# Kernel optimization log

Hardware: AMD Instinct MI355X
Metric: run time of the kernel (lower is better)

## Reference

```python
import jax, jax.numpy as jnp
import numpy as np
from jax import lax

B_, C_, H_, W_ = 4, 128, 64, 64
D_INNER, D_STATE, DT_RANK, D_CONV = 256, 16, 8, 4


def setup_inputs() -> dict:
    ks = jax.random.split(jax.random.key(0), 12)
    def rn(k, shape, fan_in):
        return jax.random.normal(k, shape, jnp.float32) * (fan_in ** -0.5)
    return {
        "x": jax.random.normal(ks[0], (B_, C_, H_, W_), jnp.float32),
        "proj_w": rn(ks[1], (C_, C_), C_),
        "in_proj_w": rn(ks[2], (2 * D_INNER, C_), C_),
        "conv_w": rn(ks[3], (D_INNER, 1, D_CONV), D_CONV),
        "conv_b": jax.random.normal(ks[4], (D_INNER,), jnp.float32) * 0.02,
        "x_proj_w": rn(ks[5], (DT_RANK + 2 * D_STATE, D_INNER), D_INNER),
        "dt_proj_w": rn(ks[6], (D_INNER, DT_RANK), DT_RANK),
        "dt_proj_b": jax.random.normal(ks[7], (D_INNER,), jnp.float32) * 0.1,
        "A_log": jax.random.uniform(ks[8], (D_INNER, D_STATE), jnp.float32),
        "D": jax.random.normal(ks[9], (D_INNER,), jnp.float32),
        "out_proj_w": rn(ks[10], (C_, D_INNER), D_INNER),
    }


def _mamba2d(x, proj_w, in_proj_w, conv_w, conv_b, x_proj_w, dt_proj_w, dt_proj_b, A_log, D, out_proj_w):
    b, c, h, w = x.shape
    L = h * w
    # 1x1 conv projection then flatten to sequence (b, L, c)
    u = jnp.einsum('oc,bchw->bohw', proj_w, x).reshape(b, c, L).transpose(0, 2, 1)
    # in_proj -> x, z gates
    xz = u @ in_proj_w.T                      # (b, L, 2*d_inner)
    xs, zg = xz[..., :D_INNER], xz[..., D_INNER:]
    # causal depthwise conv1d over sequence
    xt = xs.transpose(0, 2, 1)                # (b, d_inner, L)
    xt = lax.conv_general_dilated(xt, conv_w, window_strides=(1,),
                                  padding=[(D_CONV - 1, 0)],
                                  feature_group_count=D_INNER)
    xc = jax.nn.silu(xt + conv_b[None, :, None]).transpose(0, 2, 1)  # (b, L, d_inner)
    # input-dependent SSM params
    x_dbl = xc @ x_proj_w.T                   # (b, L, dt_rank + 2*d_state)
    dt_r = x_dbl[..., :DT_RANK]
    Bm = x_dbl[..., DT_RANK:DT_RANK + D_STATE]
    Cm = x_dbl[..., DT_RANK + D_STATE:]
    delta = jax.nn.softplus(dt_r @ dt_proj_w.T + dt_proj_b)  # (b, L, d_inner)
    A = -jnp.exp(A_log)                       # (d_inner, d_state)

    def step(hprev, inp):
        dt_t, B_t, C_t, x_t = inp             # (b,d), (b,n), (b,n), (b,d)
        dA = jnp.exp(dt_t[:, :, None] * A)    # (b, d, n)
        hn = dA * hprev + (dt_t * x_t)[:, :, None] * B_t[:, None, :]
        y = jnp.einsum('bdn,bn->bd', hn, C_t)
        return hn, y

    h0 = jnp.zeros((b, D_INNER, D_STATE), xc.dtype)
    _, ys = lax.scan(step, h0, (delta.transpose(1, 0, 2), Bm.transpose(1, 0, 2),
                                Cm.transpose(1, 0, 2), xc.transpose(1, 0, 2)))
    y = ys.transpose(1, 0, 2) + xc * D        # (b, L, d_inner) + skip
    y = y * jax.nn.silu(zg)                   # output gating
    out = y @ out_proj_w.T                    # (b, L, c)
    return out.transpose(0, 2, 1).reshape(b, c, h, w) + x


def reference(x, proj_w, in_proj_w, conv_w, conv_b, x_proj_w, dt_proj_w, dt_proj_b, A_log, D, out_proj_w):
    return _mamba2d(x, proj_w, in_proj_w, conv_w, conv_b, x_proj_w, dt_proj_w, dt_proj_b, A_log, D, out_proj_w)
```

## Files before the change

### kernel.cpp

```cpp
#include <hip/hip_runtime.h>


#define NCHUNK 128
#define CLEN 32

using s16x8 = __attribute__((ext_vector_type(8))) short;
using f32x4 = __attribute__((ext_vector_type(4))) float;

__device__ inline unsigned short f2bf(float f) {
  unsigned u = __float_as_uint(f);
  u = u + 0x7FFF + ((u >> 16) & 1);
  return (unsigned short)(u >> 16);
}

__global__ void prep_kernel(const float* __restrict__ proj_w,
                            const float* __restrict__ in_proj_w,
                            const float* __restrict__ x_proj_w,
                            const float* __restrict__ out_proj_w,
                            const float* __restrict__ A_log,
                            unsigned short* __restrict__ W2b,
                            unsigned short* __restrict__ wTb48,
                            unsigned short* __restrict__ Woutb,
                            float* __restrict__ Aneg) {
  int idx = blockIdx.x * blockDim.x + threadIdx.x;
  if (idx < 65536) {
    int o = idx >> 7, c = idx & 127;
    float acc = 0.f;
    #pragma unroll 4
    for (int i = 0; i < 128; ++i)
      acc += in_proj_w[o * 128 + i] * proj_w[i * 128 + c];
    W2b[idx] = f2bf(acc);
  } else if (idx < 65536 + 12288) {
    int t = idx - 65536;
    int j = t >> 8, k = t & 255;
    wTb48[t] = (j < 40) ? f2bf(x_proj_w[j * 256 + k]) : (unsigned short)0;
  } else if (idx < 65536 + 12288 + 32768) {
    int t = idx - (65536 + 12288);
    Woutb[t] = f2bf(out_proj_w[t]);
  } else if (idx < 65536 + 12288 + 32768 + 4096) {
    int t = idx - (65536 + 12288 + 32768);
    Aneg[t] = -__expf(A_log[t]);
  }
}

__global__ __launch_bounds__(256, 1) void gemm_xz_kernel(
    const float* __restrict__ x, const unsigned short* __restrict__ W2b,
    float* __restrict__ xz) {
  __shared__ __align__(16) unsigned short At[128 * 128];
  __shared__ __align__(16) unsigned short Bt[256 * 128];
  int m0 = (blockIdx.x >> 1) * 128;
  int o0 = (blockIdx.x & 1) * 256;
  int b  = m0 >> 12;
  int l0 = m0 & 4095;
  int t = threadIdx.x;
  #pragma unroll
  for (int j = 0; j < 16; ++j) {
    int flat = t + j * 256;
    int cr = flat >> 5, lq = (flat & 31) << 2;
    float4 v = *reinterpret_cast<const float4*>(
        &x[((size_t)(b * 128 + cr)) * 4096 + l0 + lq]);
    float vv[4] = {v.x, v.y, v.z, v.w};
    #pragma unroll
    for (int e = 0; e < 4; ++e) {
      int l = lq + e;
      int g = (cr >> 3) ^ ((l & 7) << 1);
      At[l * 128 + g * 8 + (cr & 7)] = f2bf(vv[e]);
    }
  }
  #pragma unroll
  for (int j = 0; j < 16; ++j) {
    int flat = t + j * 256;
    int row = flat >> 4, gB = flat & 15;
    s16x8 v = *reinterpret_cast<const s16x8*>(&W2b[(size_t)(o0 + row) * 128 + gB * 8]);
    int g = gB ^ ((row & 7) << 1);
    *reinterpret_cast<s16x8*>(&Bt[row * 128 + g * 8]) = v;
  }
  __syncthreads();
  int ln = t & 63, wave = t >> 6;
  int wm = wave & 1, wn = wave >> 1;
  f32x4 acc[4][8] = {};
  #pragma unroll
  for (int ks = 0; ks < 4; ++ks) {
    int gk = ks * 4 + (ln >> 4);
    s16x8 a[4], bb[8];
    #pragma unroll
    for (int mi = 0; mi < 4; ++mi) {
      int lr = wm * 64 + mi * 16 + (ln & 15);
      a[mi] = *reinterpret_cast<const s16x8*>(&At[lr * 128 + (gk ^ ((lr & 7) << 1)) * 8]);
    }
    #pragma unroll
    for (int ni = 0; ni < 8; ++ni) {
      int orow = wn * 128 + ni * 16 + (ln & 15);
      bb[ni] = *reinterpret_cast<const s16x8*>(&Bt[orow * 128 + (gk ^ ((orow & 7) << 1)) * 8]);
    }
    #pragma unroll
    for (int mi = 0; mi < 4; ++mi)
      #pragma unroll
      for (int ni = 0; ni < 8; ++ni)
        acc[mi][ni] = __builtin_amdgcn_mfma_f32_16x16x32_bf16(a[mi], bb[ni], acc[mi][ni], 0, 0, 0);
  }
  #pragma unroll
  for (int mi = 0; mi < 4; ++mi)
    #pragma unroll
    for (int ni = 0; ni < 8; ++ni)
      #pragma unroll
      for (int r = 0; r < 4; ++r) {
        int row = wm * 64 + mi * 16 + (ln >> 4) * 4 + r;
        int col = wn * 128 + ni * 16 + (ln & 15);
        xz[(size_t)(m0 + row) * 512 + o0 + col] = acc[mi][ni][r];
      }
}

__global__ __launch_bounds__(256) void conv_silu_kernel(
    const float* __restrict__ xz, const float* __restrict__ conv_w,
    const float* __restrict__ conv_b, float* __restrict__ xc,
    unsigned short* __restrict__ xcb) {
  int bl0 = blockIdx.x * 8;
  int d = threadIdx.x;
  int l0 = bl0 & 4095;
  float w0 = conv_w[d * 4 + 0], w1 = conv_w[d * 4 + 1];
  float w2 = conv_w[d * 4 + 2], w3 = conv_w[d * 4 + 3];
  float cb = conv_b[d];
  float xm1 = (l0 >= 1) ? xz[(size_t)(bl0 - 1) * 512 + d] : 0.f;
  float xm2 = (l0 >= 2) ? xz[(size_t)(bl0 - 2) * 512 + d] : 0.f;
  float xm3 = (l0 >= 3) ? xz[(size_t)(bl0 - 3) * 512 + d] : 0.f;
  #pragma unroll
  for (int r = 0; r < 8; ++r) {
    size_t bl = bl0 + r;
    float x0 = xz[bl * 512 + d];
    float acc = cb + w3 * x0 + w2 * xm1 + w1 * xm2 + w0 * xm3;
    float s = acc * (1.f / (1.f + __expf(-acc)));
    xc[bl * 256 + d] = s;
    xcb[bl * 256 + d] = f2bf(s);
    xm3 = xm2; xm2 = xm1; xm1 = x0;
  }
}

__global__ __launch_bounds__(256) void xdbl_mfma_kernel(
    const unsigned short* __restrict__ xcb, const unsigned short* __restrict__ wTb48,
    float* __restrict__ xdbl48) {
  __shared__ __align__(16) unsigned short At[64 * 256];
  __shared__ __align__(16) unsigned short Bt[48 * 256];
  int m0 = blockIdx.x * 64;
  int t = threadIdx.x;
  #pragma unroll
  for (int it = 0; it < 8; ++it) {
    int f = t + it * 256;
    int row = f >> 5, g0 = f & 31;
    s16x8 v = *reinterpret_cast<const s16x8*>(&xcb[(size_t)(m0 + row) * 256 + g0 * 8]);
    int g = g0 ^ ((row & 7) << 1);
    *reinterpret_cast<s16x8*>(&At[row * 256 + g * 8]) = v;
  }
  #pragma unroll
  for (int it = 0; it < 6; ++it) {
    int f = t + it * 256;
    int row = f >> 5, g0 = f & 31;
    s16x8 v = *reinterpret_cast<const s16x8*>(&wTb48[(size_t)row * 256 + g0 * 8]);
    int g = g0 ^ ((row & 7) << 1);
    *reinterpret_cast<s16x8*>(&Bt[row * 256 + g * 8]) = v;
  }
  __syncthreads();
  int ln = t & 63, wm = t >> 6;
  f32x4 acc[3] = {};
  #pragma unroll
  for (int ks = 0; ks < 8; ++ks) {
    int gk = ks * 4 + (ln >> 4);
    int ar = wm * 16 + (ln & 15);
    s16x8 a = *reinterpret_cast<const s16x8*>(&At[ar * 256 + (gk ^ ((ar & 7) << 1)) * 8]);
    #pragma unroll
    for (int nt = 0; nt < 3; ++nt) {
      int br = nt * 16 + (ln & 15);
      s16x8 bb = *reinterpret_cast<const s16x8*>(&Bt[br * 256 + (gk ^ ((br & 7) << 1)) * 8]);
      acc[nt] = __builtin_amdgcn_mfma_f32_16x16x32_bf16(a, bb, acc[nt], 0, 0, 0);
    }
  }
  #pragma unroll
  for (int nt = 0; nt < 3; ++nt)
    #pragma unroll
    for (int r = 0; r < 4; ++r) {
      int row = m0 + wm * 16 + (ln >> 4) * 4 + r;
      xdbl48[(size_t)row * 48 + nt * 16 + (ln & 15)] = acc[nt][r];
    }
}

__global__ __launch_bounds__(256) void scan1_kernel(
    const float* __restrict__ xc, const float* __restrict__ xdbl48,
    const float* __restrict__ dt_proj_w, const float* __restrict__ dt_proj_b,
    const float* __restrict__ Aneg,
    float* __restrict__ Ssum, float* __restrict__ chH) {
  __shared__ __align__(16) float lBC[CLEN][32];
  __shared__ __align__(16) float sdtr[CLEN][8];
  int bc = blockIdx.x;
  int b = bc >> 7;
  int bl0 = bc * 32;
  int tid = threadIdx.x;
  {
    int t0 = tid >> 3, q = (tid & 7) << 2;
    *reinterpret_cast<float4*>(&lBC[t0][q]) =
        *reinterpret_cast<const float4*>(&xdbl48[(size_t)(bl0 + t0) * 48 + 8 + q]);
    if (tid < 64) {
      int t1 = tid >> 1, q1 = (tid & 1) << 2;
      *reinterpret_cast<float4*>(&sdtr[t1][q1]) =
          *reinterpret_cast<const float4*>(&xdbl48[(size_t)(bl0 + t1) * 48 + q1]);
    }
  }
  int d = tid;
  float wrow[8];
  *reinterpret_cast<float4*>(&wrow[0]) =
      *reinterpret_cast<const float4*>(&dt_proj_w[d * 8]);
  *reinterpret_cast<float4*>(&wrow[4]) =
      *reinterpret_cast<const float4*>(&dt_proj_w[d * 8 + 4]);
  float bb = dt_proj_b[d];
  float An[16];
  #pragma unroll
  for (int q = 0; q < 4; ++q)
    *reinterpret_cast<float4*>(&An[q * 4]) =
        *reinterpret_cast<const float4*>(&Aneg[d * 16 + q * 4]);
  float xv[CLEN];
  #pragma unroll
  for (int t = 0; t < CLEN; ++t)
    xv[t] = xc[(size_t)(bl0 + t) * 256 + d];
  __syncthreads();
  float h[16] = {};
  float S = 0.f;
  #pragma unroll
  for (int t = 0; t < CLEN; ++t) {
    float a = bb;
    #pragma unroll
    for (int q = 0; q < 8; ++q) a += sdtr[t][q] * wrow[q];
    float dlv = fmaxf(a, 0.f) + __logf(1.f + __expf(-fabsf(a)));
    S += dlv;
    float dlx = dlv * xv[t];
    float4 B0 = *reinterpret_cast<const float4*>(&lBC[t][0]);
    float4 B1 = *reinterpret_cast<const float4*>(&lBC[t][4]);
    float4 B2 = *reinterpret_cast<const float4*>(&lBC[t][8]);
    float4 B3 = *reinterpret_cast<const float4*>(&lBC[t][12]);
    float Bv[16] = {B0.x,B0.y,B0.z,B0.w,B1.x,B1.y,B1.z,B1.w,
                    B2.x,B2.y,B2.z,B2.w,B3.x,B3.y,B3.z,B3.w};
    #pragma unroll
    for (int n = 0; n < 16; ++n)
      h[n] = __expf(dlv * An[n]) * h[n] + dlx * Bv[n];
  }
  int c = bc & 127;
  int p = b * 256 + d;
  Ssum[c * 1024 + p] = S;
  size_t base = ((size_t)(c * 1024 + p)) * 16;
  #pragma unroll
  for (int q = 0; q < 4; ++q) {
    float4 v{h[q*4+0], h[q*4+1], h[q*4+2], h[q*4+3]};
    *reinterpret_cast<float4*>(&chH[base + q * 4]) = v;
  }
}

__global__ void scan2_kernel(const float* __restrict__ Aneg,
                             const float* __restrict__ Ssum,
                             const float* __restrict__ chH,
                             float* __restrict__ chS) {
  int q = blockIdx.x * blockDim.x + threadIdx.x;
  int p = q >> 4, n = q & 15;
  int d = p & 255;
  float An = Aneg[d * 16 + n];
  float h = 0.f;
  #pragma unroll 8
  for (int c = 0; c < NCHUNK; ++c) {
    size_t idx = ((size_t)(c * 1024 + p)) * 16 + n;
    float S = Ssum[c * 1024 + p];
    float hl = chH[idx];
    chS[idx] = h;
    h = __expf(An * S) * h + hl;
  }
}

__global__ __launch_bounds__(256) void scan3_kernel(
    const float* __restrict__ xc, const float* __restrict__ xdbl48,
    const float* __restrict__ dt_proj_w, const float* __restrict__ dt_proj_b,
    const float* __restrict__ Aneg, const float* __restrict__ chS,
    const float* __restrict__ Dvec, const float* __restrict__ xz,
    unsigned short* __restrict__ y2b) {
  __shared__ __align__(16) float lBC[CLEN][32];
  __shared__ __align__(16) float sdtr[CLEN][8];
  int bc = blockIdx.x;
  int b = bc >> 7, c = bc & 127;
  int bl0 = bc * 32;
  int tid = threadIdx.x;
  {
    int t0 = tid >> 3, q = (tid & 7) << 2;
    *reinterpret_cast<float4*>(&lBC[t0][q]) =
        *reinterpret_cast<const float4*>(&xdbl48[(size_t)(bl0 + t0) * 48 + 8 + q]);
    if (tid < 64) {
      int t1 = tid >> 1, q1 = (tid & 1) << 2;
      *reinterpret_cast<float4*>(&sdtr[t1][q1]) =
          *reinterpret_cast<const float4*>(&xdbl48[(size_t)(bl0 + t1) * 48 + q1]);
    }
  }
  int d = tid;
  float wrow[8];
  *reinterpret_cast<float4*>(&wrow[0]) =
      *reinterpret_cast<const float4*>(&dt_proj_w[d * 8]);
  *reinterpret_cast<float4*>(&wrow[4]) =
      *reinterpret_cast<const float4*>(&dt_proj_w[d * 8 + 4]);
  float bb = dt_proj_b[d];
  float An[16];
  #pragma unroll
  for (int q = 0; q < 4; ++q)
    *reinterpret_cast<float4*>(&An[q * 4]) =
        *reinterpret_cast<const float4*>(&Aneg[d * 16 + q * 4]);
  int p = b * 256 + d;
  float h[16];
  {
    size_t base = ((size_t)(c * 1024 + p)) * 16;
    #pragma unroll
    for (int q = 0; q < 4; ++q) {
      float4 v = *reinterpret_cast<const float4*>(&chS[base + q * 4]);
      h[q*4+0] = v.x; h[q*4+1] = v.y; h[q*4+2] = v.z; h[q*4+3] = v.w;
    }
  }
  float xv[CLEN], zv[CLEN];
  #pragma unroll
  for (int t = 0; t < CLEN; ++t) {
    xv[t] = xc[(size_t)(bl0 + t) * 256 + d];
    zv[t] = xz[(size_t)(bl0 + t) * 512 + 256 + d];
  }
  float Dd = Dvec[d];
  __syncthreads();
  #pragma unroll
  for (int t = 0; t < CLEN; ++t) {
    float a = bb;
    #pragma unroll
    for (int q = 0; q < 8; ++q) a += sdtr[t][q] * wrow[q];
    float dlv = fmaxf(a, 0.f) + __logf(1.f + __expf(-fabsf(a)));
    float xvv = xv[t];
    float dlx = dlv * xvv;
    float4 B0 = *reinterpret_cast<const float4*>(&lBC[t][0]);
    float4 B1 = *reinterpret_cast<const float4*>(&lBC[t][4]);
    float4 B2 = *reinterpret_cast<const float4*>(&lBC[t][8]);
    float4 B3 = *reinterpret_cast<const float4*>(&lBC[t][12]);
    float4 C0 = *reinterpret_cast<const float4*>(&lBC[t][16]);
    float4 C1 = *reinterpret_cast<const float4*>(&lBC[t][20]);
    float4 C2 = *reinterpret_cast<const float4*>(&lBC[t][24]);
    float4 C3 = *reinterpret_cast<const float4*>(&lBC[t][28]);
    float Bv[16] = {B0.x,B0.y,B0.z,B0.w,B1.x,B1.y,B1.z,B1.w,
                    B2.x,B2.y,B2.z,B2.w,B3.x,B3.y,B3.z,B3.w};
    float Cv[16] = {C0.x,C0.y,C0.z,C0.w,C1.x,C1.y,C1.z,C1.w,
                    C2.x,C2.y,C2.z,C2.w,C3.x,C3.y,C3.z,C3.w};
    float y = 0.f;
    #pragma unroll
    for (int n = 0; n < 16; ++n) {
      h[n] = __expf(dlv * An[n]) * h[n] + dlx * Bv[n];
      y += h[n] * Cv[n];
    }
    float z = zv[t];
    float sil = z * (1.f / (1.f + __expf(-z)));
    y2b[(size_t)(bl0 + t) * 256 + d] = f2bf((y + xvv * Dd) * sil);
  }
}

__global__ __launch_bounds__(256) void gemm_out_kernel(
    const unsigned short* __restrict__ y2b, const unsigned short* __restrict__ Woutb,
    const float* __restrict__ x, float* __restrict__ out) {
  __shared__ __align__(16) unsigned short At[64 * 256];
  __shared__ __align__(16) unsigned short Bt[128 * 256];
  int m0 = blockIdx.x * 64;
  int b = m0 >> 12, l0 = m0 & 4095;
  int t = threadIdx.x;
  #pragma unroll
  for (int it = 0; it < 8; ++it) {
    int f = t + it * 256;
    int row = f >> 5, g0 = f & 31;
    s16x8 v = *reinterpret_cast<const s16x8*>(&y2b[(size_t)(m0 + row) * 256 + g0 * 8]);
    int g = g0 ^ ((row & 7) << 1);
    *reinterpret_cast<s16x8*>(&At[row * 256 + g * 8]) = v;
  }
  #pragma unroll
  for (int it = 0; it < 16; ++it) {
    int f = t + it * 256;
    int row = f >> 5, g0 = f & 31;
    s16x8 v = *reinterpret_cast<const s16x8*>(&Woutb[(size_t)row * 256 + g0 * 8]);
    int g = g0 ^ ((row & 7) << 1);
    *reinterpret_cast<s16x8*>(&Bt[row * 256 + g * 8]) = v;
  }
  __syncthreads();
  int ln = t & 63, wm = t >> 6;
  f32x4 acc[8] = {};
  #pragma unroll
  for (int ks = 0; ks < 8; ++ks) {
    int gk = ks * 4 + (ln >> 4);
    int ar = wm * 16 + (ln & 15);
    s16x8 a = *reinterpret_cast<const s16x8*>(&At[ar * 256 + (gk ^ ((ar & 7) << 1)) * 8]);
    #pragma unroll
    for (int nt = 0; nt < 8; ++nt) {
      int br = nt * 16 + (ln & 15);
      s16x8 bb = *reinterpret_cast<const s16x8*>(&Bt[br * 256 + (gk ^ ((br & 7) << 1)) * 8]);
      acc[nt] = __builtin_amdgcn_mfma_f32_16x16x32_bf16(a, bb, acc[nt], 0, 0, 0);
    }
  }
  #pragma unroll
  for (int nt = 0; nt < 8; ++nt) {
    int cc = nt * 16 + (ln & 15);
    size_t base = ((size_t)(b * 128 + cc)) * 4096 + l0 + wm * 16 + ((ln >> 4) << 2);
    float4 xr = *reinterpret_cast<const float4*>(&x[base]);
    float4 o{acc[nt][0] + xr.x, acc[nt][1] + xr.y, acc[nt][2] + xr.z, acc[nt][3] + xr.w};
    *reinterpret_cast<float4*>(&out[base]) = o;
  }
}

extern "C" void kernel_launch(void* const* d_in, const int* in_sizes, int n_in,
                              void* d_out, int out_size, void* d_ws, size_t ws_size,
                              hipStream_t stream) {
  const float* x         = (const float*)d_in[0];
  const float* proj_w    = (const float*)d_in[1];
  const float* in_proj_w = (const float*)d_in[2];
  const float* conv_w    = (const float*)d_in[3];
  const float* conv_b    = (const float*)d_in[4];
  const float* x_proj_w  = (const float*)d_in[5];
  const float* dt_proj_w = (const float*)d_in[6];
  const float* dt_proj_b = (const float*)d_in[7];
  const float* A_log     = (const float*)d_in[8];
  const float* Dvec      = (const float*)d_in[9];
  const float* out_proj_w= (const float*)d_in[10];

  float* ws = (float*)d_ws;
  float*          Aneg   = ws;
  unsigned short* W2b    = (unsigned short*)(ws + 4096);
  unsigned short* wTb48  = (unsigned short*)(ws + 36864);
  unsigned short* Woutb  = (unsigned short*)(ws + 43008);
  float*          xz     = ws + 59392;
  float*          xc     = xz + 8388608;
  unsigned short* xcb    = (unsigned short*)(xc + 4194304);
  float*          xdbl48 = xc + 4194304 + 2097152;
  float*          Ssum   = xdbl48 + 786432;
  float*          chH    = Ssum + 131072;
  float*          chS    = chH + 2097152;
  unsigned short* y2b    = (unsigned short*)(chS + 2097152);
  float* out = (float*)d_out;

  prep_kernel<<<448, 256, 0, stream>>>(proj_w, in_proj_w, x_proj_w, out_proj_w, A_log,
                                       W2b, wTb48, Woutb, Aneg);
  gemm_xz_kernel<<<256, 256, 0, stream>>>(x, W2b, xz);
  conv_silu_kernel<<<2048, 256, 0, stream>>>(xz, conv_w, conv_b, xc, xcb);
  xdbl_mfma_kernel<<<256, 256, 0, stream>>>(xcb, wTb48, xdbl48);
  scan1_kernel<<<512, 256, 0, stream>>>(xc, xdbl48, dt_proj_w, dt_proj_b, Aneg, Ssum, chH);
  scan2_kernel<<<64, 256, 0, stream>>>(Aneg, Ssum, chH, chS);
  scan3_kernel<<<512, 256, 0, stream>>>(xc, xdbl48, dt_proj_w, dt_proj_b, Aneg, chS,
                                        Dvec, xz, y2b);
  gemm_out_kernel<<<256, 256, 0, stream>>>(y2b, Woutb, x, out);
}
```

Before: 185.0 us.

## Halve scan chunk length and store chunk carry states in bf16

Cuts the chunked selective scan's chunk length from 32 to 16, doubling the number of chunks and blocks in the first and third scan passes so more workgroups run in parallel. Carry states passed between scan passes are now stored as packed bf16 instead of fp32, which halves that intermediate traffic. In exchange the serial inter-chunk pass walks twice as many chunks, and the bf16 carries lose precision in the recurrent state.

```diff
diff --git a/kernel.cpp b/kernel.cpp
--- a/kernel.cpp
+++ b/kernel.cpp
@@ -1,8 +1,8 @@
 #include <hip/hip_runtime.h>
 
 
-#define NCHUNK 128
-#define CLEN 32
+#define NCHUNK 256
+#define CLEN 16
 
 using s16x8 = __attribute__((ext_vector_type(8))) short;
 using f32x4 = __attribute__((ext_vector_type(4))) float;
@@ -12,6 +12,8 @@
   u = u + 0x7FFF + ((u >> 16) & 1);
   return (unsigned short)(u >> 16);
 }
+__device__ inline float bf2f_lo(unsigned v) { return __uint_as_float(v << 16); }
+__device__ inline float bf2f_hi(unsigned v) { return __uint_as_float(v & 0xFFFF0000u); }
 
 __global__ void prep_kernel(const float* __restrict__ proj_w,
                             const float* __restrict__ in_proj_w,
@@ -187,22 +189,22 @@
     const float* __restrict__ xc, const float* __restrict__ xdbl48,
     const float* __restrict__ dt_proj_w, const float* __restrict__ dt_proj_b,
     const float* __restrict__ Aneg,
-    float* __restrict__ Ssum, float* __restrict__ chH) {
+    float* __restrict__ Ssum, unsigned* __restrict__ chHb) {
   __shared__ __align__(16) float lBC[CLEN][32];
   __shared__ __align__(16) float sdtr[CLEN][8];
   int bc = blockIdx.x;
-  int b = bc >> 7;
-  int bl0 = bc * 32;
+  int b = bc >> 8, c = bc & 255;
+  int bl0 = bc * CLEN;
   int tid = threadIdx.x;
-  {
+  if (tid < 128) {
     int t0 = tid >> 3, q = (tid & 7) << 2;
     *reinterpret_cast<float4*>(&lBC[t0][q]) =
         *reinterpret_cast<const float4*>(&xdbl48[(size_t)(bl0 + t0) * 48 + 8 + q]);
-    if (tid < 64) {
-      int t1 = tid >> 1, q1 = (tid & 1) << 2;
-      *reinterpret_cast<float4*>(&sdtr[t1][q1]) =
-          *reinterpret_cast<const float4*>(&xdbl48[(size_t)(bl0 + t1) * 48 + q1]);
-    }
+  }
+  if (tid < 32) {
+    int t1 = tid >> 1, q1 = (tid & 1) << 2;
+    *reinterpret_cast<float4*>(&sdtr[t1][q1]) =
+        *reinterpret_cast<const float4*>(&xdbl48[(size_t)(bl0 + t1) * 48 + q1]);
   }
   int d = tid;
   float wrow[8];
@@ -241,21 +243,21 @@
     for (int n = 0; n < 16; ++n)
       h[n] = __expf(dlv * An[n]) * h[n] + dlx * Bv[n];
   }
-  int c = bc & 127;
   int p = b * 256 + d;
   Ssum[c * 1024 + p] = S;
-  size_t base = ((size_t)(c * 1024 + p)) * 16;
-  #pragma unroll
-  for (int q = 0; q < 4; ++q) {
-    float4 v{h[q*4+0], h[q*4+1], h[q*4+2], h[q*4+3]};
-    *reinterpret_cast<float4*>(&chH[base + q * 4]) = v;
-  }
+  unsigned up[8];
+  #pragma unroll
+  for (int q = 0; q < 8; ++q)
+    up[q] = (unsigned)f2bf(h[2 * q]) | ((unsigned)f2bf(h[2 * q + 1]) << 16);
+  size_t ub = ((size_t)(c * 1024 + p)) * 8;
+  *reinterpret_cast<uint4*>(&chHb[ub])     = uint4{up[0], up[1], up[2], up[3]};
+  *reinterpret_cast<uint4*>(&chHb[ub + 4]) = uint4{up[4], up[5], up[6], up[7]};
 }
 
 __global__ void scan2_kernel(const float* __restrict__ Aneg,
                              const float* __restrict__ Ssum,
-                             const float* __restrict__ chH,
-                             float* __restrict__ chS) {
+                             const unsigned short* __restrict__ chHb,
+                             unsigned short* __restrict__ chSb) {
   int q = blockIdx.x * blockDim.x + threadIdx.x;
   int p = q >> 4, n = q & 15;
   int d = p & 255;
@@ -265,8 +267,8 @@
   for (int c = 0; c < NCHUNK; ++c) {
     size_t idx = ((size_t)(c * 1024 + p)) * 16 + n;
     float S = Ssum[c * 1024 + p];
-    float hl = chH[idx];
-    chS[idx] = h;
+    float hl = bf2f_lo((unsigned)chHb[idx]);
+    chSb[idx] = f2bf(h);
     h = __expf(An * S) * h + hl;
   }
 }
@@ -274,24 +276,24 @@
 __global__ __launch_bounds__(256) void scan3_kernel(
     const float* __restrict__ xc, const float* __restrict__ xdbl48,
     const float* __restrict__ dt_proj_w, const float* __restrict__ dt_proj_b,
-    const float* __restrict__ Aneg, const float* __restrict__ chS,
+    const float* __restrict__ Aneg, const unsigned* __restrict__ chSb,
     const float* __restrict__ Dvec, const float* __restrict__ xz,
     unsigned short* __restrict__ y2b) {
   __shared__ __align__(16) float lBC[CLEN][32];
   __shared__ __align__(16) float sdtr[CLEN][8];
   int bc = blockIdx.x;
-  int b = bc >> 7, c = bc & 127;
-  int bl0 = bc * 32;
+  int b = bc >> 8, c = bc & 255;
+  int bl0 = bc * CLEN;
   int tid = threadIdx.x;
-  {
+  if (tid < 128) {
     int t0 = tid >> 3, q = (tid & 7) << 2;
     *reinterpret_cast<float4*>(&lBC[t0][q]) =
         *reinterpret_cast<const float4*>(&xdbl48[(size_t)(bl0 + t0) * 48 + 8 + q]);
-    if (tid < 64) {
-      int t1 = tid >> 1, q1 = (tid & 1) << 2;
-      *reinterpret_cast<float4*>(&sdtr[t1][q1]) =
-          *reinterpret_cast<const float4*>(&xdbl48[(size_t)(bl0 + t1) * 48 + q1]);
-    }
+  }
+  if (tid < 32) {
+    int t1 = tid >> 1, q1 = (tid & 1) << 2;
+    *reinterpret_cast<float4*>(&sdtr[t1][q1]) =
+        *reinterpret_cast<const float4*>(&xdbl48[(size_t)(bl0 + t1) * 48 + q1]);
   }
   int d = tid;
   float wrow[8];
@@ -308,12 +310,17 @@
   int p = b * 256 + d;
   float h[16];
   {
-    size_t base = ((size_t)(c * 1024 + p)) * 16;
-    #pragma unroll
-    for (int q = 0; q < 4; ++q) {
-      float4 v = *reinterpret_cast<const float4*>(&chS[base + q * 4]);
-      h[q*4+0] = v.x; h[q*4+1] = v.y; h[q*4+2] = v.z; h[q*4+3] = v.w;
-    }
+    size_t ub = ((size_t)(c * 1024 + p)) * 8;
+    uint4 s0 = *reinterpret_cast<const uint4*>(&chSb[ub]);
+    uint4 s1 = *reinterpret_cast<const uint4*>(&chSb[ub + 4]);
+    h[0] = bf2f_lo(s0.x); h[1] = bf2f_hi(s0.x);
+    h[2] = bf2f_lo(s0.y); h[3] = bf2f_hi(s0.y);
+    h[4] = bf2f_lo(s0.z); h[5] = bf2f_hi(s0.z);
+    h[6] = bf2f_lo(s0.w); h[7] = bf2f_hi(s0.w);
+    h[8] = bf2f_lo(s1.x); h[9] = bf2f_hi(s1.x);
+    h[10] = bf2f_lo(s1.y); h[11] = bf2f_hi(s1.y);
+    h[12] = bf2f_lo(s1.z); h[13] = bf2f_hi(s1.z);
+    h[14] = bf2f_lo(s1.w); h[15] = bf2f_hi(s1.w);
   }
   float xv[CLEN], zv[CLEN];
   #pragma unroll
@@ -429,9 +436,9 @@
   unsigned short* xcb    = (unsigned short*)(xc + 4194304);
   float*          xdbl48 = xc + 4194304 + 2097152;
   float*          Ssum   = xdbl48 + 786432;
-  float*          chH    = Ssum + 131072;
-  float*          chS    = chH + 2097152;
-  unsigned short* y2b    = (unsigned short*)(chS + 2097152);
+  unsigned*       chHb   = (unsigned*)(Ssum + 262144);
+  unsigned*       chSb   = chHb + 2097152;
+  unsigned short* y2b    = (unsigned short*)(chSb + 2097152);
   float* out = (float*)d_out;
 
   prep_kernel<<<448, 256, 0, stream>>>(proj_w, in_proj_w, x_proj_w, out_proj_w, A_log,
@@ -439,9 +446,11 @@
   gemm_xz_kernel<<<256, 256, 0, stream>>>(x, W2b, xz);
   conv_silu_kernel<<<2048, 256, 0, stream>>>(xz, conv_w, conv_b, xc, xcb);
   xdbl_mfma_kernel<<<256, 256, 0, stream>>>(xcb, wTb48, xdbl48);
-  scan1_kernel<<<512, 256, 0, stream>>>(xc, xdbl48, dt_proj_w, dt_proj_b, Aneg, Ssum, chH);
-  scan2_kernel<<<64, 256, 0, stream>>>(Aneg, Ssum, chH, chS);
-  scan3_kernel<<<512, 256, 0, stream>>>(xc, xdbl48, dt_proj_w, dt_proj_b, Aneg, chS,
-                                        Dvec, xz, y2b);
+  scan1_kernel<<<1024, 256, 0, stream>>>(xc, xdbl48, dt_proj_w, dt_proj_b, Aneg,
+                                         Ssum, chHb);
+  scan2_kernel<<<64, 256, 0, stream>>>(Aneg, Ssum, (const unsigned short*)chHb,
+                                       (unsigned short*)chSb);
+  scan3_kernel<<<1024, 256, 0, stream>>>(xc, xdbl48, dt_proj_w, dt_proj_b, Aneg,
+                                         chSb, Dvec, xz, y2b);
   gemm_out_kernel<<<256, 256, 0, stream>>>(y2b, Woutb, x, out);
 }
```

After: 181.3 us. 1.02x faster.

## Store x/z and conv output as transposed bf16 for vectorized per-channel reads

Applied to the files above, without the earlier changes.

The in-projection GEMM now writes x and z as bf16 in a channel-major (b, d, L) layout instead of fp32 row-major xz. The conv and scan kernels read contiguous 16-byte vectors per channel rather than strided scalar loads. Outputs of conv and scan3 are staged through shared memory so their row-major stores are coalesced. This cuts intermediate memory traffic by about half and improves coalescing, at the cost of bf16 rounding of x, z and xc inside the scan, which adds accuracy risk.

```diff
diff --git a/kernel.cpp b/kernel.cpp
--- a/kernel.cpp
+++ b/kernel.cpp
@@ -11,6 +11,9 @@
   unsigned u = __float_as_uint(f);
   u = u + 0x7FFF + ((u >> 16) & 1);
   return (unsigned short)(u >> 16);
+}
+__device__ inline float bfu(unsigned short v) {
+  return __uint_as_float((unsigned)v << 16);
 }
 
 __global__ void prep_kernel(const float* __restrict__ proj_w,
@@ -45,7 +48,7 @@
 
 __global__ __launch_bounds__(256, 1) void gemm_xz_kernel(
     const float* __restrict__ x, const unsigned short* __restrict__ W2b,
-    float* __restrict__ xz) {
+    unsigned short* __restrict__ xT, unsigned short* __restrict__ zT) {
   __shared__ __align__(16) unsigned short At[128 * 128];
   __shared__ __align__(16) unsigned short Bt[256 * 128];
   int m0 = (blockIdx.x >> 1) * 128;
@@ -99,40 +102,65 @@
       for (int ni = 0; ni < 8; ++ni)
         acc[mi][ni] = __builtin_amdgcn_mfma_f32_16x16x32_bf16(a[mi], bb[ni], acc[mi][ni], 0, 0, 0);
   }
+  unsigned short* T = (o0 == 0) ? xT : zT;
   #pragma unroll
   for (int mi = 0; mi < 4; ++mi)
     #pragma unroll
-    for (int ni = 0; ni < 8; ++ni)
-      #pragma unroll
-      for (int r = 0; r < 4; ++r) {
-        int row = wm * 64 + mi * 16 + (ln >> 4) * 4 + r;
-        int col = wn * 128 + ni * 16 + (ln & 15);
-        xz[(size_t)(m0 + row) * 512 + o0 + col] = acc[mi][ni][r];
-      }
+    for (int ni = 0; ni < 8; ++ni) {
+      int colg = wn * 128 + ni * 16 + (ln & 15);
+      int lrow = l0 + wm * 64 + mi * 16 + ((ln >> 4) << 2);
+      ushort4 h4{f2bf(acc[mi][ni][0]), f2bf(acc[mi][ni][1]),
+                 f2bf(acc[mi][ni][2]), f2bf(acc[mi][ni][3])};
+      *reinterpret_cast<ushort4*>(&T[((size_t)(b * 256 + colg)) * 4096 + lrow]) = h4;
+    }
 }
 
 __global__ __launch_bounds__(256) void conv_silu_kernel(
-    const float* __restrict__ xz, const float* __restrict__ conv_w,
-    const float* __restrict__ conv_b, float* __restrict__ xc,
+    const unsigned short* __restrict__ xT, const float* __restrict__ conv_w,
+    const float* __restrict__ conv_b, unsigned short* __restrict__ xcT,
     unsigned short* __restrict__ xcb) {
-  int bl0 = blockIdx.x * 8;
+  __shared__ unsigned short sxc[16][256];
+  int blk = blockIdx.x;
+  int b = blk >> 8, ch = blk & 255;
+  int l0 = ch * 16;
   int d = threadIdx.x;
-  int l0 = bl0 & 4095;
+  size_t rowbase = ((size_t)(b * 256 + d)) * 4096;
+  s16x8 w16[3];
+  const s16x8* src = reinterpret_cast<const s16x8*>(&xT[rowbase + l0 - 8]);
+  w16[0] = src[0]; w16[1] = src[1]; w16[2] = src[2];
+  float wf[24];
+  #pragma unroll
+  for (int i = 0; i < 3; ++i)
+    #pragma unroll
+    for (int e = 0; e < 8; ++e)
+      wf[i * 8 + e] = bfu((unsigned short)w16[i][e]);
+  if (l0 == 0) { wf[5] = 0.f; wf[6] = 0.f; wf[7] = 0.f; }
   float w0 = conv_w[d * 4 + 0], w1 = conv_w[d * 4 + 1];
   float w2 = conv_w[d * 4 + 2], w3 = conv_w[d * 4 + 3];
   float cb = conv_b[d];
-  float xm1 = (l0 >= 1) ? xz[(size_t)(bl0 - 1) * 512 + d] : 0.f;
-  float xm2 = (l0 >= 2) ? xz[(size_t)(bl0 - 2) * 512 + d] : 0.f;
-  float xm3 = (l0 >= 3) ? xz[(size_t)(bl0 - 3) * 512 + d] : 0.f;
-  #pragma unroll
-  for (int r = 0; r < 8; ++r) {
-    size_t bl = bl0 + r;
-    float x0 = xz[bl * 512 + d];
-    float acc = cb + w3 * x0 + w2 * xm1 + w1 * xm2 + w0 * xm3;
+  unsigned short outv[16];
+  #pragma unroll
+  for (int r = 0; r < 16; ++r) {
+    float acc = cb + w3 * wf[8 + r] + w2 * wf[7 + r] + w1 * wf[6 + r] + w0 * wf[5 + r];
     float s = acc * (1.f / (1.f + __expf(-acc)));
-    xc[bl * 256 + d] = s;
-    xcb[bl * 256 + d] = f2bf(s);
-    xm3 = xm2; xm2 = xm1; xm1 = x0;
+    unsigned short v = f2bf(s);
+    outv[r] = v;
+    sxc[r][d] = v;
+  }
+  #pragma unroll
+  for (int i = 0; i < 2; ++i) {
+    s16x8 v;
+    #pragma unroll
+    for (int e = 0; e < 8; ++e) v[e] = (short)outv[i * 8 + e];
+    *reinterpret_cast<s16x8*>(&xcT[rowbase + l0 + i * 8]) = v;
+  }
+  __syncthreads();
+  #pragma unroll
+  for (int it = 0; it < 2; ++it) {
+    int idx = d + it * 256;
+    int l = idx >> 5, ds8 = (idx & 31) * 8;
+    s16x8 v = *reinterpret_cast<const s16x8*>(&sxc[l][ds8]);
+    *reinterpret_cast<s16x8*>(&xcb[((size_t)(b * 4096 + l0 + l)) * 256 + ds8]) = v;
   }
 }
 
@@ -184,15 +212,15 @@
 }
 
 __global__ __launch_bounds__(256) void scan1_kernel(
-    const float* __restrict__ xc, const float* __restrict__ xdbl48,
+    const unsigned short* __restrict__ xcT, const float* __restrict__ xdbl48,
     const float* __restrict__ dt_proj_w, const float* __restrict__ dt_proj_b,
     const float* __restrict__ Aneg,
     float* __restrict__ Ssum, float* __restrict__ chH) {
   __shared__ __align__(16) float lBC[CLEN][32];
   __shared__ __align__(16) float sdtr[CLEN][8];
-  int bc = blockIdx.x;
-  int b = bc >> 7;
-  int bl0 = bc * 32;
+  int blk = blockIdx.x;
+  int b = blk >> 7, c = blk & 127;
+  int bl0 = blk * CLEN;
   int tid = threadIdx.x;
   {
     int t0 = tid >> 3, q = (tid & 7) << 2;
@@ -206,20 +234,20 @@
   }
   int d = tid;
   float wrow[8];
-  *reinterpret_cast<float4*>(&wrow[0]) =
-      *reinterpret_cast<const float4*>(&dt_proj_w[d * 8]);
-  *reinterpret_cast<float4*>(&wrow[4]) =
-      *reinterpret_cast<const float4*>(&dt_proj_w[d * 8 + 4]);
+  *reinterpret_cast<float4*>(&wrow[0]) = *reinterpret_cast<const float4*>(&dt_proj_w[d * 8]);
+  *reinterpret_cast<float4*>(&wrow[4]) = *reinterpret_cast<const float4*>(&dt_proj_w[d * 8 + 4]);
   float bb = dt_proj_b[d];
   float An[16];
   #pragma unroll
   for (int q = 0; q < 4; ++q)
     *reinterpret_cast<float4*>(&An[q * 4]) =
         *reinterpret_cast<const float4*>(&Aneg[d * 16 + q * 4]);
-  float xv[CLEN];
-  #pragma unroll
-  for (int t = 0; t < CLEN; ++t)
-    xv[t] = xc[(size_t)(bl0 + t) * 256 + d];
+  s16x8 xw[4];
+  {
+    const s16x8* src = reinterpret_cast<const s16x8*>(
+        &xcT[((size_t)(b * 256 + d)) * 4096 + c * CLEN]);
+    xw[0] = src[0]; xw[1] = src[1]; xw[2] = src[2]; xw[3] = src[3];
+  }
   __syncthreads();
   float h[16] = {};
   float S = 0.f;
@@ -230,18 +258,11 @@
     for (int q = 0; q < 8; ++q) a += sdtr[t][q] * wrow[q];
     float dlv = fmaxf(a, 0.f) + __logf(1.f + __expf(-fabsf(a)));
     S += dlv;
-    float dlx = dlv * xv[t];
-    float4 B0 = *reinterpret_cast<const float4*>(&lBC[t][0]);
-    float4 B1 = *reinterpret_cast<const float4*>(&lBC[t][4]);
-    float4 B2 = *reinterpret_cast<const float4*>(&lBC[t][8]);
-    float4 B3 = *reinterpret_cast<const float4*>(&lBC[t][12]);
-    float Bv[16] = {B0.x,B0.y,B0.z,B0.w,B1.x,B1.y,B1.z,B1.w,
-                    B2.x,B2.y,B2.z,B2.w,B3.x,B3.y,B3.z,B3.w};
+    float dlx = dlv * bfu((unsigned short)xw[t >> 3][t & 7]);
     #pragma unroll
     for (int n = 0; n < 16; ++n)
-      h[n] = __expf(dlv * An[n]) * h[n] + dlx * Bv[n];
-  }
-  int c = bc & 127;
+      h[n] = __expf(dlv * An[n]) * h[n] + dlx * lBC[t][n];
+  }
   int p = b * 256 + d;
   Ssum[c * 1024 + p] = S;
   size_t base = ((size_t)(c * 1024 + p)) * 16;
@@ -272,16 +293,17 @@
 }
 
 __global__ __launch_bounds__(256) void scan3_kernel(
-    const float* __restrict__ xc, const float* __restrict__ xdbl48,
+    const unsigned short* __restrict__ xcT, const unsigned short* __restrict__ zT,
+    const float* __restrict__ xdbl48,
     const float* __restrict__ dt_proj_w, const float* __restrict__ dt_proj_b,
     const float* __restrict__ Aneg, const float* __restrict__ chS,
-    const float* __restrict__ Dvec, const float* __restrict__ xz,
-    unsigned short* __restrict__ y2b) {
+    const float* __restrict__ Dvec, unsigned short* __restrict__ y2b) {
   __shared__ __align__(16) float lBC[CLEN][32];
   __shared__ __align__(16) float sdtr[CLEN][8];
-  int bc = blockIdx.x;
-  int b = bc >> 7, c = bc & 127;
-  int bl0 = bc * 32;
+  __shared__ unsigned short sy[CLEN][256];
+  int blk = blockIdx.x;
+  int b = blk >> 7, c = blk & 127;
+  int bl0 = blk * CLEN;
   int tid = threadIdx.x;
   {
     int t0 = tid >> 3, q = (tid & 7) << 2;
@@ -295,10 +317,8 @@
   }
   int d = tid;
   float wrow[8];
-  *reinterpret_cast<float4*>(&wrow[0]) =
-      *reinterpret_cast<const float4*>(&dt_proj_w[d * 8]);
-  *reinterpret_cast<float4*>(&wrow[4]) =
-      *reinterpret_cast<const float4*>(&dt_proj_w[d * 8 + 4]);
+  *reinterpret_cast<float4*>(&wrow[0]) = *reinterpret_cast<const float4*>(&dt_proj_w[d * 8]);
+  *reinterpret_cast<float4*>(&wrow[4]) = *reinterpret_cast<const float4*>(&dt_proj_w[d * 8 + 4]);
   float bb = dt_proj_b[d];
   float An[16];
   #pragma unroll
@@ -315,11 +335,13 @@
       h[q*4+0] = v.x; h[q*4+1] = v.y; h[q*4+2] = v.z; h[q*4+3] = v.w;
     }
   }
-  float xv[CLEN], zv[CLEN];
-  #pragma unroll
-  for (int t = 0; t < CLEN; ++t) {
-    xv[t] = xc[(size_t)(bl0 + t) * 256 + d];
-    zv[t] = xz[(size_t)(bl0 + t) * 512 + 256 + d];
+  s16x8 xw[4], zw[4];
+  {
+    size_t rb = ((size_t)(b * 256 + d)) * 4096 + c * CLEN;
+    const s16x8* sx = reinterpret_cast<const s16x8*>(&xcT[rb]);
+    const s16x8* sz = reinterpret_cast<const s16x8*>(&zT[rb]);
+    xw[0] = sx[0]; xw[1] = sx[1]; xw[2] = sx[2]; xw[3] = sx[3];
+    zw[0] = sz[0]; zw[1] = sz[1]; zw[2] = sz[2]; zw[3] = sz[3];
   }
   float Dd = Dvec[d];
   __syncthreads();
@@ -329,29 +351,25 @@
     #pragma unroll
     for (int q = 0; q < 8; ++q) a += sdtr[t][q] * wrow[q];
     float dlv = fmaxf(a, 0.f) + __logf(1.f + __expf(-fabsf(a)));
-    float xvv = xv[t];
-    float dlx = dlv * xvv;
-    float4 B0 = *reinterpret_cast<const float4*>(&lBC[t][0]);
-    float4 B1 = *reinterpret_cast<const float4*>(&lBC[t][4]);
-    float4 B2 = *reinterpret_cast<const float4*>(&lBC[t][8]);
-    float4 B3 = *reinterpret_cast<const float4*>(&lBC[t][12]);
-    float4 C0 = *reinterpret_cast<const float4*>(&lBC[t][16]);
-    float4 C1 = *reinterpret_cast<const float4*>(&lBC[t][20]);
-    float4 C2 = *reinterpret_cast<const float4*>(&lBC[t][24]);
-    float4 C3 = *reinterpret_cast<const float4*>(&lBC[t][28]);
-    float Bv[16] = {B0.x,B0.y,B0.z,B0.w,B1.x,B1.y,B1.z,B1.w,
-                    B2.x,B2.y,B2.z,B2.w,B3.x,B3.y,B3.z,B3.w};
-    float Cv[16] = {C0.x,C0.y,C0.z,C0.w,C1.x,C1.y,C1.z,C1.w,
-                    C2.x,C2.y,C2.z,C2.w,C3.x,C3.y,C3.z,C3.w};
+    float xval = bfu((unsigned short)xw[t >> 3][t & 7]);
+    float dlx = dlv * xval;
     float y = 0.f;
     #pragma unroll
     for (int n = 0; n < 16; ++n) {
-      h[n] = __expf(dlv * An[n]) * h[n] + dlx * Bv[n];
-      y += h[n] * Cv[n];
-    }
-    float z = zv[t];
+      h[n] = __expf(dlv * An[n]) * h[n] + dlx * lBC[t][n];
+      y += h[n] * lBC[t][16 + n];
+    }
+    float z = bfu((unsigned short)zw[t >> 3][t & 7]);
     float sil = z * (1.f / (1.f + __expf(-z)));
-    y2b[(size_t)(bl0 + t) * 256 + d] = f2bf((y + xvv * Dd) * sil);
+    sy[t][d] = f2bf((y + xval * Dd) * sil);
+  }
+  __syncthreads();
+  #pragma unroll
+  for (int it = 0; it < 4; ++it) {
+    int idx = tid + it * 256;
+    int l = idx >> 5, ds8 = (idx & 31) * 8;
+    s16x8 v = *reinterpret_cast<const s16x8*>(&sy[l][ds8]);
+    *reinterpret_cast<s16x8*>(&y2b[((size_t)(bl0 + l)) * 256 + ds8]) = v;
   }
 }
 
@@ -424,24 +442,26 @@
   unsigned short* W2b    = (unsigned short*)(ws + 4096);
   unsigned short* wTb48  = (unsigned short*)(ws + 36864);
   unsigned short* Woutb  = (unsigned short*)(ws + 43008);
-  float*          xz     = ws + 59392;
-  float*          xc     = xz + 8388608;
-  unsigned short* xcb    = (unsigned short*)(xc + 4194304);
-  float*          xdbl48 = xc + 4194304 + 2097152;
-  float*          Ssum   = xdbl48 + 786432;
-  float*          chH    = Ssum + 131072;
-  float*          chS    = chH + 2097152;
-  unsigned short* y2b    = (unsigned short*)(chS + 2097152);
+  unsigned short* xT     = (unsigned short*)(ws + 59424);
+  unsigned short* zT     = (unsigned short*)(ws + 2156576);
+  unsigned short* xcT    = (unsigned short*)(ws + 4253728);
+  unsigned short* xcb    = (unsigned short*)(ws + 6350880);
+  float*          xdbl48 = ws + 8448032;
+  float*          Ssum   = ws + 9234464;
+  float*          chH    = ws + 9365536;
+  float*          chS    = ws + 11462688;
+  unsigned short* y2b    = (unsigned short*)(ws + 13559840);
   float* out = (float*)d_out;
 
   prep_kernel<<<448, 256, 0, stream>>>(proj_w, in_proj_w, x_proj_w, out_proj_w, A_log,
                                        W2b, wTb48, Woutb, Aneg);
-  gemm_xz_kernel<<<256, 256, 0, stream>>>(x, W2b, xz);
-  conv_silu_kernel<<<2048, 256, 0, stream>>>(xz, conv_w, conv_b, xc, xcb);
+  gemm_xz_kernel<<<256, 256, 0, stream>>>(x, W2b, xT, zT);
+  conv_silu_kernel<<<1024, 256, 0, stream>>>(xT, conv_w, conv_b, xcT, xcb);
   xdbl_mfma_kernel<<<256, 256, 0, stream>>>(xcb, wTb48, xdbl48);
-  scan1_kernel<<<512, 256, 0, stream>>>(xc, xdbl48, dt_proj_w, dt_proj_b, Aneg, Ssum, chH);
+  scan1_kernel<<<512, 256, 0, stream>>>(xcT, xdbl48, dt_proj_w, dt_proj_b, Aneg,
+                                        Ssum, chH);
   scan2_kernel<<<64, 256, 0, stream>>>(Aneg, Ssum, chH, chS);
-  scan3_kernel<<<512, 256, 0, stream>>>(xc, xdbl48, dt_proj_w, dt_proj_b, Aneg, chS,
-                                        Dvec, xz, y2b);
+  scan3_kernel<<<512, 256, 0, stream>>>(xcT, zT, xdbl48, dt_proj_w, dt_proj_b, Aneg,
+                                        chS, Dvec, y2b);
   gemm_out_kernel<<<256, 256, 0, stream>>>(y2b, Woutb, x, out);
 }
```

Result: no change. 184.1 us (-0.5%).
